# Kernel optimization log

Hardware: AMD Instinct MI355X
Metric: run time of the kernel (lower is better)

Reference implementation:

```python
import jax, jax.numpy as jnp
import numpy as np

K = 1.0        # Lorentz curvature parameter
SQRT_K = 1.0
B, E, T = 128, 64, 2048
F1, D, F2, NC = 16, 2, 32, 4


def linner(u, v):
    # Lorentz inner product <u,v>_L over the last axis (time component first)
    return -u[..., :1] * v[..., :1] + jnp.sum(u[..., 1:] * v[..., 1:], axis=-1, keepdims=True)


def add_time(space):
    # manifold.add_time / projx: time = sqrt(K + ||space||^2)
    t = jnp.sqrt(K + jnp.sum(space * space, axis=-1, keepdims=True))
    return jnp.concatenate([t, space], axis=-1)


def conv2d(x, w, padding, groups=1):
    return jax.lax.conv_general_dilated(
        x, w, window_strides=(1, 1), padding=padding,
        dimension_numbers=('NCHW', 'OIHW', 'NCHW'), feature_group_count=groups)


def bn2d(x, gamma, beta, eps=1e-3):
    # BatchNorm2d (training-mode batch statistics, eps=0.001)
    mean = jnp.mean(x, axis=(0, 2, 3), keepdims=True)
    var = jnp.var(x, axis=(0, 2, 3), keepdims=True)
    return (x - mean) * jax.lax.rsqrt(var + eps) * gamma.reshape(1, -1, 1, 1) + beta.reshape(1, -1, 1, 1)


def avgpool_w(x, k=4):
    # torch AvgPool2d((1,k), stride=k), floor mode
    Wo = x.shape[-1] // k
    return jnp.mean(x[..., :Wo * k].reshape(x.shape[:-1] + (Wo, k)), axis=-1)


def lorentz_bn(x, s, eps=1e-5):
    # AdaMom-style Riemannian batch norm on the hyperboloid (eta=1 -> pure batch stats,
    # learn_mean=False -> target mean is origin, learn_std=True -> learnable scale s).
    C = x.shape[-1]
    o = jnp.zeros((C,), x.dtype).at[0].set(SQRT_K)                      # origin
    avg = jnp.mean(x, axis=0, keepdims=True)
    mu = SQRT_K * avg / jnp.sqrt(jnp.maximum(-linner(avg, avg), 1e-8))  # batch centroid
    xin = -linner(x, mu)                                                # >= K on manifold
    dist = SQRT_K * jnp.arccosh(jnp.maximum(xin / K, 1.0 + 1e-7))
    u = x - (xin / K) * mu                                              # log_mu direction
    v = dist * u / jnp.sqrt(jnp.maximum(linner(u, u), 1e-8))            # log_mu(x)
    var = jnp.mean(dist * dist, axis=0, keepdims=True)                  # scalar dispersion
    v = v + (linner(o, v) / (K - linner(mu, o))) * (mu + o)             # PT mu -> origin
    v = v * (s.reshape(1, 1, -1, 1) / jnp.sqrt(var + eps))
    n = jnp.sqrt(jnp.maximum(linner(v, v), 1e-9))
    return jnp.cosh(n / SQRT_K) * o + SQRT_K * jnp.sinh(n / SQRT_K) * v / n  # exp_origin


def lorentz_avgpool_w(x, k=4):
    # window mean followed by Lorentz centroid renormalization
    Bb, H, W, C = x.shape
    Wo = W // k
    avg = jnp.mean(x[:, :, :Wo * k, :].reshape(Bb, H, Wo, k, C), axis=3)
    return SQRT_K * avg / jnp.sqrt(jnp.maximum(-linner(avg, avg), 1e-8))


def lorentz_flatten(x):
    Bb, H, W, C = x.shape
    t = x[..., 0].reshape(Bb, -1)
    s = x[..., 1:].reshape(Bb, -1)
    t_new = jnp.sqrt(jnp.maximum(jnp.sum(t * t, axis=-1, keepdims=True) - (H * W - 1) * K, 1e-8))
    return jnp.concatenate([t_new, s], axis=-1)


def lorentz_mlr(x, a, z):
    inv = 1.0 / SQRT_K
    norm_z = jnp.linalg.norm(z, axis=-1)                                  # (NC,)
    w_t = jnp.sinh(inv * a) * norm_z
    beta = jnp.sqrt(jnp.maximum((jnp.cosh(inv * a) * norm_z) ** 2 - w_t ** 2, 1e-8))
    alpha = -x[:, :1] * w_t[None, :] + jnp.cosh(inv * a)[None, :] * (x[:, 1:] @ z.T)
    d = SQRT_K * jnp.abs(jnp.arcsinh(inv * alpha / beta[None, :]))
    return jnp.sign(alpha) * beta[None, :] * d


def setup_inputs():
    key = jax.random.key(0)
    ks = jax.random.split(key, 8)
    Cin = F1 * D + 1   # 33
    Cout = F2 + 1      # 33
    feat = F2 * 128    # flattened space dim: W 2049 -> 512 -> 513 -> 128
    return {
        'inputs': jax.random.normal(ks[0], (B, E, T), jnp.float32),
        'domains': jax.random.randint(ks[1], (B,), 0, 4, jnp.int32),
        'conv1_w': jax.random.normal(ks[2], (F1, 1, 1, 32), jnp.float32) / np.float32(np.sqrt(32.0)),
        'bn1_gamma': jnp.ones((F1,), jnp.float32),
        'bn1_beta': jnp.zeros((F1,), jnp.float32),
        'conv2_w': jax.random.normal(ks[3], (F1 * D, 1, E, 1), jnp.float32) / np.float32(np.sqrt(E)),
        'bn2_gamma': jnp.ones((F1 * D,), jnp.float32),
        'bn2_beta': jnp.zeros((F1 * D,), jnp.float32),
        'ec1_w': jax.random.normal(ks[4], (F1 * D, 1, 1, 16), jnp.float32) / np.float32(np.sqrt(16.0)),
        'lc1_w': jax.random.normal(ks[5], (Cout, Cin), jnp.float32) / np.float32(np.sqrt(Cin)),
        'bn_s': jnp.ones((513,), jnp.float32),
        'mlr_a': jax.random.normal(ks[6], (NC,), jnp.float32) * 0.01,
        'mlr_z': jax.random.normal(ks[7], (NC, feat), jnp.float32) * 0.01,
    }


def reference(inputs, domains, conv1_w, bn1_gamma, bn1_beta, conv2_w, bn2_gamma, bn2_beta,
              ec1_w, lc1_w, bn_s, mlr_a, mlr_z):
    x = inputs[:, None, :, :]                           # (B,1,E,T)
    x = conv2d(x, conv1_w, [(0, 0), (16, 16)])          # (B,16,64,2049)
    x = bn2d(x, bn1_gamma, bn1_beta)
    x = conv2d(x, conv2_w, [(0, 0), (0, 0)], groups=F1) # (B,32,1,2049) depthwise over electrodes
    x = bn2d(x, bn2_gamma, bn2_beta)
    x = jax.nn.elu(x)
    x = avgpool_w(x)                                    # (B,32,1,512)  (dropout = eval no-op)
    x = conv2d(x, ec1_w, [(0, 0), (8, 8)], groups=F1 * D)  # (B,32,1,513)
    x = jnp.transpose(x, (0, 2, 3, 1))                  # (B,1,513,32) channels-last
    x = x / (jnp.linalg.norm(x, axis=-1, keepdims=True) + 1e-8)
    x = add_time(x)                                     # projx(pad(x, (1,0))) -> (B,1,513,33)
    # LorentzConv2d 1x1 (kernel_len=1): clamp time, linear, recompute time from space output
    pre = jnp.concatenate([jnp.maximum(x[..., :1], SQRT_K), x[..., 1:]], axis=-1)
    y = jnp.einsum('bhwi,oi->bhwo', pre, lc1_w)
    x = add_time(y[..., 1:])
    x = lorentz_bn(x, bn_s)
    x = add_time(jax.nn.elu(x[..., 1:]))                # LorentzeLU
    x = lorentz_avgpool_w(x)                            # (B,1,128,33)
    feats = lorentz_flatten(x)                          # (B, 4097)
    logits = lorentz_mlr(feats, mlr_a, mlr_z)           # (B, 4)
    return logits, feats
```

## Files before the change

kernel.cpp:

```cpp
#include <hip/hip_runtime.h>
#include <math.h>

#define BB 128
#define EE 64
#define TT 2048
#define C2 32
#define W1 2049
#define WPW 512
#define FEAT 4096
#define NBLK 1024

#define OFF_P    ((size_t)0)
#define OFF_X2   ((size_t)4194304)
#define OFF_PSUM ((size_t)8388608)
#define OFF_PSQ  ((size_t)8421376)
#define OFF_SS   ((size_t)8454144)
#define OFF_ZZ   ((size_t)8454208)
#define OFF_QSQ  ((size_t)10551360)

__device__ __forceinline__ unsigned short f2b(float f) {
    unsigned int u = __float_as_uint(f);
    u += 0x7FFFu + ((u >> 16) & 1u);
    return (unsigned short)(u >> 16);
}
__device__ __forceinline__ float b2f(unsigned short s) {
    return __uint_as_float(((unsigned int)s) << 16);
}

__global__ __launch_bounds__(256) void k_p(const float* __restrict__ in,
        const float* __restrict__ w2, unsigned short* __restrict__ P) {
    int b = blockIdx.y, t0 = blockIdx.x * 256, tid = threadIdx.x;
    __shared__ unsigned short li[64][256];
    __shared__ float lw2s[32][64];
    const float* ib = in + (size_t)b * EE * TT + t0;
    for (int j = tid; j < 64 * 64; j += 256) {
        int e = j >> 6, q = j & 63;
        float4 v = *(const float4*)(ib + e * TT + q * 4);
        li[e][q * 4 + 0] = f2b(v.x); li[e][q * 4 + 1] = f2b(v.y);
        li[e][q * 4 + 2] = f2b(v.z); li[e][q * 4 + 3] = f2b(v.w);
    }
    for (int j = tid; j < 2048; j += 256) lw2s[j >> 6][j & 63] = w2[j];
    __syncthreads();
    int cg = tid >> 6, colg = tid & 63;
    int c8 = cg * 8;
    float acc[4][8];
#pragma unroll
    for (int x = 0; x < 4; x++)
#pragma unroll
        for (int jj = 0; jj < 8; jj++) acc[x][jj] = 0.f;
    for (int e = 0; e < 64; e += 2) {
        uint2 r0 = *(const uint2*)&li[e][colg * 4];
        uint2 r1 = *(const uint2*)&li[e + 1][colg * 4];
        float v0[4], v1[4];
        v0[0] = __uint_as_float(r0.x << 16); v0[1] = __uint_as_float(r0.x & 0xFFFF0000u);
        v0[2] = __uint_as_float(r0.y << 16); v0[3] = __uint_as_float(r0.y & 0xFFFF0000u);
        v1[0] = __uint_as_float(r1.x << 16); v1[1] = __uint_as_float(r1.x & 0xFFFF0000u);
        v1[2] = __uint_as_float(r1.y << 16); v1[3] = __uint_as_float(r1.y & 0xFFFF0000u);
#pragma unroll
        for (int jj = 0; jj < 8; jj++) {
            float2 wv = *(const float2*)&lw2s[c8 + jj][e];
#pragma unroll
            for (int x = 0; x < 4; x++) {
                acc[x][jj] = fmaf(wv.x, v0[x], acc[x][jj]);
                acc[x][jj] = fmaf(wv.y, v1[x], acc[x][jj]);
            }
        }
    }
    unsigned short* Pb = P + (size_t)b * C2 * TT + t0 + colg * 4;
#pragma unroll
    for (int jj = 0; jj < 8; jj++) {
        int c = c8 + jj;
        uint2 o;
        o.x = (unsigned int)f2b(acc[0][jj]) | ((unsigned int)f2b(acc[1][jj]) << 16);
        o.y = (unsigned int)f2b(acc[2][jj]) | ((unsigned int)f2b(acc[3][jj]) << 16);
        *(uint2*)(Pb + (size_t)c * TT) = o;
    }
}

__global__ __launch_bounds__(256) void k_cs(const unsigned short* __restrict__ P,
        const float* __restrict__ w1, const float* __restrict__ g1,
        unsigned short* __restrict__ x2, float* __restrict__ psum, float* __restrict__ psq) {
    int bx = blockIdx.x, b = blockIdx.y, w0 = bx * 256, tid = threadIdx.x;
    __shared__ unsigned short lp[32][288];
    __shared__ float lw1[16][32];
    __shared__ float lds_s[32], lds_q[32];
    const unsigned short* Pb = P + (size_t)b * C2 * TT;
    for (int j = tid; j < 32 * 72; j += 256) {
        int c = j / 72, g4 = j % 72;
        int t = w0 - 16 + g4 * 4;
        uint2 v = make_uint2(0u, 0u);
        if (t >= 0 && t + 3 < TT) v = *(const uint2*)(Pb + (size_t)c * TT + t);
        *(uint2*)&lp[c][g4 * 4] = v;
    }
    for (int j = tid; j < 512; j += 256) {
        int g = j >> 5;
        float sgn = (g1[g] < 0.f) ? -1.f : 1.f;
        lw1[g][j & 31] = w1[j] * sgn;
    }
    __syncthreads();
    for (int r = 0; r < 8; r++) {
        int task = r * 256 + tid;
        int c = task >> 6;
        int wq = task & 63;
        int wbase = wq * 4;
        float win[36];
#pragma unroll
        for (int i = 0; i < 9; i++) {
            uint2 v = *(const uint2*)&lp[c][wbase + i * 4];
            win[i * 4 + 0] = __uint_as_float(v.x << 16);
            win[i * 4 + 1] = __uint_as_float(v.x & 0xFFFF0000u);
            win[i * 4 + 2] = __uint_as_float(v.y << 16);
            win[i * 4 + 3] = __uint_as_float(v.y & 0xFFFF0000u);
        }
        const float* wc = lw1[c >> 1];
        float ls = 0.f, lq = 0.f;
        float accs[4];
#pragma unroll
        for (int i = 0; i < 4; i++) {
            float acc = 0.f;
#pragma unroll
            for (int k = 0; k < 32; k++) acc = fmaf(wc[k], win[i + k], acc);
            accs[i] = acc;
            ls += acc; lq = fmaf(acc, acc, lq);
        }
        uint2 o;
        o.x = (unsigned int)f2b(accs[0]) | ((unsigned int)f2b(accs[1]) << 16);
        o.y = (unsigned int)f2b(accs[2]) | ((unsigned int)f2b(accs[3]) << 16);
        *(uint2*)(x2 + ((size_t)b * C2 + c) * TT + w0 + wbase) = o;
#pragma unroll
        for (int d = 1; d < 64; d <<= 1) {
            ls += __shfl_xor(ls, d);
            lq += __shfl_xor(lq, d);
        }
        if ((tid & 63) == 0) { lds_s[c] = ls; lds_q[c] = lq; }
    }
    __syncthreads();
    if (bx == 7 && tid < 32) {
        const float* wc = lw1[tid >> 1];
        float acc = 0.f;
#pragma unroll
        for (int k = 0; k < 16; k++) acc = fmaf(wc[k], b2f(lp[tid][256 + k]), acc);
        lds_s[tid] += acc;
        lds_q[tid] += acc * acc;
    }
    __syncthreads();
    if (tid < 32) {
        int blk = b * 8 + bx;
        psum[tid * NBLK + blk] = lds_s[tid];
        psq[tid * NBLK + blk]  = lds_q[tid];
    }
}

__global__ __launch_bounds__(64) void k_bn2fin(
        const float* __restrict__ psum, const float* __restrict__ psq,
        const float* __restrict__ gamma, const float* __restrict__ beta,
        float* __restrict__ ss) {
    int c = blockIdx.x, l = threadIdx.x;
    float s = 0.f, q = 0.f;
    for (int j = l; j < NBLK; j += 64) { s += psum[c * NBLK + j]; q += psq[c * NBLK + j]; }
#pragma unroll
    for (int d = 1; d < 64; d <<= 1) { s += __shfl_xor(s, d); q += __shfl_xor(q, d); }
    if (l == 0) {
        float n = (float)(BB * W1);
        float m = s / n;
        float var = q / n - m * m;
        float sc = gamma[c] * rsqrtf(var + 1e-3f);
        ss[c] = sc;
        ss[32 + c] = beta[c] - m * sc;
    }
}

__global__ __launch_bounds__(256) void k_mid(
        const unsigned short* __restrict__ x2, const float* __restrict__ ss,
        const float* __restrict__ ew, float* __restrict__ zz) {
    int b = blockIdx.y, w0 = blockIdx.x * 64, tid = threadIdx.x;
    __shared__ unsigned short lx[32][324];
    __shared__ float ly[32][82];
    __shared__ float lss[64];
    __shared__ float lew[32][17];
    const unsigned short* xb = x2 + (size_t)b * C2 * TT;
    int base_t = 4 * w0 - 32;
    for (int it = 0; it < 10; it++) {
        int idx = it * 256 + tid;
        int c = idx / 80, q = idx - c * 80;
        int t0 = base_t + q * 4;
        uint2 v = make_uint2(0u, 0u);
        if (t0 >= 0 && t0 <= TT - 4) v = *(const uint2*)(xb + (size_t)c * TT + t0);
        *(uint2*)&lx[c][q * 4] = v;
    }
    if (tid < 64) lss[tid] = ss[tid];
    for (int j = tid; j < 512; j += 256) lew[j >> 4][j & 15] = ew[j];
    __syncthreads();
    for (int it = 0; it < 10; it++) {
        int idx = it * 256 + tid;
        int c = idx & 31, j2 = idx >> 5;
        int ty = w0 - 8 + j2;
        float r = 0.f;
        if (ty >= 0 && ty < WPW) {
            uint2 v = *(const uint2*)&lx[c][j2 * 4];
            float sc = lss[c], sh = lss[32 + c];
            float a0 = fmaf(sc, __uint_as_float(v.x << 16), sh);
            float a1 = fmaf(sc, __uint_as_float(v.x & 0xFFFF0000u), sh);
            float a2 = fmaf(sc, __uint_as_float(v.y << 16), sh);
            float a3 = fmaf(sc, __uint_as_float(v.y & 0xFFFF0000u), sh);
            r = ((a0 > 0.f) ? a0 : expm1f(a0)) + ((a1 > 0.f) ? a1 : expm1f(a1))
              + ((a2 > 0.f) ? a2 : expm1f(a2)) + ((a3 > 0.f) ? a3 : expm1f(a3));
            r *= 0.25f;
        }
        ly[c][j2] = r;
    }
    __syncthreads();
    int c = tid & 31, wl = tid >> 5;
    float win[24];
#pragma unroll
    for (int m = 0; m < 12; m++) {
        float2 v = *(const float2*)&ly[c][wl * 8 + m * 2];
        win[m * 2] = v.x; win[m * 2 + 1] = v.y;
    }
    float wc[16];
#pragma unroll
    for (int k = 0; k < 16; k++) wc[k] = lew[c][k];
    float* zb = zz + ((size_t)(w0 + wl * 8) * BB + b) * C2 + c;
#pragma unroll
    for (int i = 0; i < 8; i++) {
        float acc = 0.f;
#pragma unroll
        for (int k = 0; k < 16; k++) acc = fmaf(wc[k], win[i + k], acc);
        zb[(size_t)i * BB * C2] = acc;
    }
}

__global__ __launch_bounds__(512) void k_tail(
        const float* __restrict__ zz, const float* __restrict__ lc1,
        const float* __restrict__ bs, float* __restrict__ outp,
        float* __restrict__ qsq) {
    int wp = blockIdx.x;
    int tid = threadIdx.x;
    int j = tid >> 7;
    int b = tid & 127;
    int w = wp * 4 + j;
    __shared__ float lws[33][32];
    __shared__ float lwt[33];
    __shared__ float wsum[4][2][33];
    __shared__ float vred[4][2];
    __shared__ float lavg[128][33];
    for (int i = tid; i < 1089; i += 512) {
        int o = i / 33, ii = i - o * 33;
        float v = lc1[i];
        if (ii == 0) lwt[o] = v; else lws[o][ii - 1] = v;
    }
    float* lz = &lavg[0][0];
    for (int i = tid; i < 128 * 33; i += 512) lz[i] = 0.f;
    __syncthreads();
    float x[33];
    {
        float xin[32];
        float ssq = 0.f;
        const float* zp = zz + ((size_t)w * BB + b) * C2;
#pragma unroll
        for (int i = 0; i < 32; i += 4) {
            float4 v = *(const float4*)(zp + i);
            xin[i] = v.x; xin[i + 1] = v.y; xin[i + 2] = v.z; xin[i + 3] = v.w;
        }
#pragma unroll
        for (int i = 0; i < 32; i++) ssq = fmaf(xin[i], xin[i], ssq);
        float inv = 1.f / (sqrtf(ssq) + 1e-8f);
        float s2 = 0.f;
#pragma unroll
        for (int i = 0; i < 32; i++) { xin[i] *= inv; s2 = fmaf(xin[i], xin[i], s2); }
        float t = sqrtf(1.f + s2);
        float pre0 = fmaxf(t, 1.f);
        float sy = 0.f;
        for (int o = 1; o < 33; o++) {
            float a = lwt[o] * pre0;
#pragma unroll
            for (int q4 = 0; q4 < 8; q4++) {
                float4 wv = *(const float4*)&lws[o][q4 * 4];
                a = fmaf(wv.x, xin[q4 * 4 + 0], a);
                a = fmaf(wv.y, xin[q4 * 4 + 1], a);
                a = fmaf(wv.z, xin[q4 * 4 + 2], a);
                a = fmaf(wv.w, xin[q4 * 4 + 3], a);
            }
            x[o] = a;
            sy = fmaf(a, a, sy);
        }
        x[0] = sqrtf(1.f + sy);
    }
    float mu[33];
#pragma unroll
    for (int ch = 0; ch < 33; ch++) {
        float s = x[ch];
        s += __shfl_xor(s, 1);  s += __shfl_xor(s, 2);  s += __shfl_xor(s, 4);
        s += __shfl_xor(s, 8);  s += __shfl_xor(s, 16); s += __shfl_xor(s, 32);
        mu[ch] = s;
    }
    int wv = b >> 6;
    if ((b & 63) == 0) {
#pragma unroll
        for (int ch = 0; ch < 33; ch++) wsum[j][wv][ch] = mu[ch];
    }
    __syncthreads();
#pragma unroll
    for (int ch = 0; ch < 33; ch++) mu[ch] = (wsum[j][0][ch] + wsum[j][1][ch]) * (1.f / 128.f);
    float a0 = mu[0], sp = 0.f;
#pragma unroll
    for (int i = 1; i < 33; i++) sp = fmaf(mu[i], mu[i], sp);
    float rd = rsqrtf(fmaxf(a0 * a0 - sp, 1e-8f));
#pragma unroll
    for (int ch = 0; ch < 33; ch++) mu[ch] *= rd;
    float xin2 = x[0] * mu[0];
#pragma unroll
    for (int i = 1; i < 33; i++) xin2 -= x[i] * mu[i];
    float dist = acoshf(fmaxf(xin2, 1.f + 1e-7f));
    float dq = dist * dist;
    dq += __shfl_xor(dq, 1);  dq += __shfl_xor(dq, 2);  dq += __shfl_xor(dq, 4);
    dq += __shfl_xor(dq, 8);  dq += __shfl_xor(dq, 16); dq += __shfl_xor(dq, 32);
    if ((b & 63) == 0) vred[j][wv] = dq;
    __syncthreads();
    float var = (vred[j][0] + vred[j][1]) * (1.f / 128.f);
#pragma unroll
    for (int ch = 0; ch < 33; ch++) x[ch] = x[ch] - xin2 * mu[ch];
    float lu = -x[0] * x[0];
#pragma unroll
    for (int i = 1; i < 33; i++) lu = fmaf(x[i], x[i], lu);
    float f = dist * rsqrtf(fmaxf(lu, 1e-8f));
#pragma unroll
    for (int ch = 0; ch < 33; ch++) x[ch] *= f;
    float corr = -x[0] / (1.f + mu[0]);
    x[0] += corr * (mu[0] + 1.f);
#pragma unroll
    for (int i = 1; i < 33; i++) x[i] = fmaf(corr, mu[i], x[i]);
    float scb = bs[w] * rsqrtf(var + 1e-5f);
#pragma unroll
    for (int ch = 0; ch < 33; ch++) x[ch] *= scb;
    float nn = -x[0] * x[0];
#pragma unroll
    for (int i = 1; i < 33; i++) nn = fmaf(x[i], x[i], nn);
    float n = sqrtf(fmaxf(nn, 1e-9f));
    float shn = sinhf(n) / n;
    float sg = 0.f;
#pragma unroll
    for (int i = 1; i < 33; i++) {
        float e = shn * x[i];
        e = (e > 0.f) ? e : expm1f(e);
        x[i] = e;
        sg = fmaf(e, e, sg);
    }
    x[0] = sqrtf(1.f + sg);
    for (int jj = 0; jj < 4; jj++) {
        if (j == jj) {
#pragma unroll
            for (int ch = 0; ch < 33; ch++) lavg[b][ch] += x[ch];
        }
        __syncthreads();
    }
    if (tid < 128) {
        int bb2 = tid;
        float avg[33];
#pragma unroll
        for (int ch = 0; ch < 33; ch++) avg[ch] = lavg[bb2][ch] * 0.25f;
        float sp2 = 0.f;
#pragma unroll
        for (int i = 1; i < 33; i++) sp2 = fmaf(avg[i], avg[i], sp2);
        float l = avg[0] * avg[0] - sp2;
        float rd2 = rsqrtf(fmaxf(l, 1e-8f));
        float q0 = avg[0] * rd2;
        float* fb = outp + 512 + (size_t)bb2 * 4097;
#pragma unroll
        for (int i = 1; i < 33; i++) fb[1 + wp * 32 + (i - 1)] = avg[i] * rd2;
        qsq[bb2 * 128 + wp] = q0 * q0;
    }
}

__global__ __launch_bounds__(256) void k_mlr2(
        const float* __restrict__ qsq, const float* __restrict__ z,
        const float* __restrict__ a, float* __restrict__ outp) {
    int b = blockIdx.x, tid = threadIdx.x;
    __shared__ float red[4][8];
    __shared__ float tnsh;
    if (tid < 64) {
        float s = qsq[b * 128 + tid] + qsq[b * 128 + 64 + tid];
#pragma unroll
        for (int d = 1; d < 64; d <<= 1) s += __shfl_xor(s, d);
        if (tid == 0) tnsh = sqrtf(fmaxf(s - 127.f, 1e-8f));
    }
    __syncthreads();
    float tn = tnsh;
    const float* fs = outp + 512 + (size_t)b * 4097 + 1;
    float sdot[4] = {0.f, 0.f, 0.f, 0.f}, sq[4] = {0.f, 0.f, 0.f, 0.f};
    for (int i = tid * 4; i < FEAT; i += 1024) {
        float f0 = fs[i], f1 = fs[i + 1], f2 = fs[i + 2], f3 = fs[i + 3];
#pragma unroll
        for (int c = 0; c < 4; c++) {
            float4 zv = *(const float4*)(z + c * FEAT + i);
            sdot[c] = fmaf(f0, zv.x, sdot[c]); sdot[c] = fmaf(f1, zv.y, sdot[c]);
            sdot[c] = fmaf(f2, zv.z, sdot[c]); sdot[c] = fmaf(f3, zv.w, sdot[c]);
            sq[c] = fmaf(zv.x, zv.x, sq[c]); sq[c] = fmaf(zv.y, zv.y, sq[c]);
            sq[c] = fmaf(zv.z, zv.z, sq[c]); sq[c] = fmaf(zv.w, zv.w, sq[c]);
        }
    }
#pragma unroll
    for (int d = 1; d < 64; d <<= 1) {
#pragma unroll
        for (int c = 0; c < 4; c++) {
            sdot[c] += __shfl_xor(sdot[c], d);
            sq[c]   += __shfl_xor(sq[c], d);
        }
    }
    int wv = tid >> 6;
    if ((tid & 63) == 0) {
#pragma unroll
        for (int c = 0; c < 4; c++) { red[wv][c] = sdot[c]; red[wv][4 + c] = sq[c]; }
    }
    __syncthreads();
    if (tid == 0) {
        outp[512 + (size_t)b * 4097] = tn;
#pragma unroll
        for (int c = 0; c < 4; c++) {
            float dot = red[0][c] + red[1][c] + red[2][c] + red[3][c];
            float qz  = red[0][4 + c] + red[1][4 + c] + red[2][4 + c] + red[3][4 + c];
            float nz = sqrtf(qz);
            float ca = coshf(a[c]), sa = sinhf(a[c]);
            float wt = sa * nz;
            float cb = ca * nz;
            float bb = sqrtf(fmaxf(cb * cb - wt * wt, 1e-8f));
            float alpha = fmaf(-tn, wt, ca * dot);
            float d = fabsf(asinhf(alpha / bb));
            float sg = (alpha > 0.f) ? 1.f : ((alpha < 0.f) ? -1.f : 0.f);
            outp[b * 4 + c] = sg * bb * d;
        }
    }
}

extern "C" void kernel_launch(void* const* d_in, const int* in_sizes, int n_in,
                              void* d_out, int out_size, void* d_ws, size_t ws_size,
                              hipStream_t stream) {
    const float* in   = (const float*)d_in[0];
    const float* w1   = (const float*)d_in[2];
    const float* g1   = (const float*)d_in[3];
    const float* w2   = (const float*)d_in[5];
    const float* g2   = (const float*)d_in[6];
    const float* b2   = (const float*)d_in[7];
    const float* ew   = (const float*)d_in[8];
    const float* lc1  = (const float*)d_in[9];
    const float* bs   = (const float*)d_in[10];
    const float* mlra = (const float*)d_in[11];
    const float* mlrz = (const float*)d_in[12];
    float* out = (float*)d_out;
    float* ws = (float*)d_ws;

    unsigned short* P  = (unsigned short*)(ws + OFF_P);
    unsigned short* X2 = (unsigned short*)(ws + OFF_X2);
    float* PSUM = ws + OFF_PSUM;
    float* PSQ  = ws + OFF_PSQ;
    float* SS   = ws + OFF_SS;
    float* ZZ   = ws + OFF_ZZ;
    float* QSQ  = ws + OFF_QSQ;

    k_p<<<dim3(8, 128), 256, 0, stream>>>(in, w2, P);
    k_cs<<<dim3(8, 128), 256, 0, stream>>>(P, w1, g1, X2, PSUM, PSQ);
    k_bn2fin<<<32, 64, 0, stream>>>(PSUM, PSQ, g2, b2, SS);
    k_mid<<<dim3(8, 128), 256, 0, stream>>>(X2, SS, ew, ZZ);
    k_tail<<<128, 512, 0, stream>>>(ZZ, lc1, bs, out, QSQ);
    k_mlr2<<<128, 256, 0, stream>>>(QSQ, mlrz, mlra, out);
}
```

Before: 208.9 us.

## Fuse channel normalization and Lorentz 1x1 conv into the mid kernel

Result: faster. 203.6 us (-2.5%).

```diff
diff --git a/kernel.cpp b/kernel.cpp
--- a/kernel.cpp
+++ b/kernel.cpp
@@ -15,8 +15,8 @@
 #define OFF_PSUM ((size_t)8388608)
 #define OFF_PSQ  ((size_t)8421376)
 #define OFF_SS   ((size_t)8454144)
-#define OFF_ZZ   ((size_t)8454208)
-#define OFF_QSQ  ((size_t)10551360)
+#define OFF_H    ((size_t)8454208)
+#define OFF_QSQ  ((size_t)10616896)
 
 __device__ __forceinline__ unsigned short f2b(float f) {
     unsigned int u = __float_as_uint(f);
@@ -172,12 +172,15 @@
 
 __global__ __launch_bounds__(256) void k_mid(
         const unsigned short* __restrict__ x2, const float* __restrict__ ss,
-        const float* __restrict__ ew, float* __restrict__ zz) {
+        const float* __restrict__ ew, const float* __restrict__ lc1,
+        float* __restrict__ H) {
     int b = blockIdx.y, w0 = blockIdx.x * 64, tid = threadIdx.x;
     __shared__ unsigned short lx[32][324];
     __shared__ float ly[32][82];
     __shared__ float lss[64];
     __shared__ float lew[32][17];
+    __shared__ float lc[1089];
+    __shared__ float lxn[8][32];
     const unsigned short* xb = x2 + (size_t)b * C2 * TT;
     int base_t = 4 * w0 - 32;
     for (int it = 0; it < 10; it++) {
@@ -190,6 +193,7 @@
     }
     if (tid < 64) lss[tid] = ss[tid];
     for (int j = tid; j < 512; j += 256) lew[j >> 4][j & 15] = ew[j];
+    for (int j = tid; j < 1089; j += 256) lc[j] = lc1[j];
     __syncthreads();
     for (int it = 0; it < 10; it++) {
         int idx = it * 256 + tid;
@@ -220,72 +224,68 @@
     float wc[16];
 #pragma unroll
     for (int k = 0; k < 16; k++) wc[k] = lew[c][k];
-    float* zb = zz + ((size_t)(w0 + wl * 8) * BB + b) * C2 + c;
+    float acc[8];
 #pragma unroll
     for (int i = 0; i < 8; i++) {
-        float acc = 0.f;
-#pragma unroll
-        for (int k = 0; k < 16; k++) acc = fmaf(wc[k], win[i + k], acc);
-        zb[(size_t)i * BB * C2] = acc;
+        float a = 0.f;
+#pragma unroll
+        for (int k = 0; k < 16; k++) a = fmaf(wc[k], win[i + k], a);
+        acc[i] = a;
+    }
+    float wt0 = lc[(c + 1) * 33];
+    float wreg[32];
+#pragma unroll
+    for (int k = 0; k < 32; k++) wreg[k] = lc[(c + 1) * 33 + 1 + k];
+    float* lrow = lxn[wl];
+#pragma unroll 1
+    for (int i = 0; i < 8; i++) {
+        float v = acc[i];
+        float ssq = v * v;
+        ssq += __shfl_xor(ssq, 1);  ssq += __shfl_xor(ssq, 2);
+        ssq += __shfl_xor(ssq, 4);  ssq += __shfl_xor(ssq, 8);
+        ssq += __shfl_xor(ssq, 16);
+        float inv = 1.f / (sqrtf(ssq) + 1e-8f);
+        float xn = v * inv;
+        float s2 = ssq * inv * inv;
+        float pre0 = fmaxf(sqrtf(1.f + s2), 1.f);
+        lrow[c] = xn;
+        float y = wt0 * pre0;
+#pragma unroll
+        for (int q = 0; q < 8; q++) {
+            float4 xv = *(const float4*)&lrow[q * 4];
+            y = fmaf(wreg[q * 4 + 0], xv.x, y);
+            y = fmaf(wreg[q * 4 + 1], xv.y, y);
+            y = fmaf(wreg[q * 4 + 2], xv.z, y);
+            y = fmaf(wreg[q * 4 + 3], xv.w, y);
+        }
+        float sy = y * y;
+        sy += __shfl_xor(sy, 1);  sy += __shfl_xor(sy, 2);
+        sy += __shfl_xor(sy, 4);  sy += __shfl_xor(sy, 8);
+        sy += __shfl_xor(sy, 16);
+        int w = w0 + wl * 8 + i;
+        float* hrow = H + ((size_t)w * BB + b) * 33;
+        hrow[1 + c] = y;
+        if (c == 0) hrow[0] = sqrtf(1.f + sy);
     }
 }
 
 __global__ __launch_bounds__(512) void k_tail(
-        const float* __restrict__ zz, const float* __restrict__ lc1,
-        const float* __restrict__ bs, float* __restrict__ outp,
-        float* __restrict__ qsq) {
+        const float* __restrict__ H, const float* __restrict__ bs,
+        float* __restrict__ outp, float* __restrict__ qsq) {
     int wp = blockIdx.x;
     int tid = threadIdx.x;
     int j = tid >> 7;
     int b = tid & 127;
     int w = wp * 4 + j;
-    __shared__ float lws[33][32];
-    __shared__ float lwt[33];
     __shared__ float wsum[4][2][33];
     __shared__ float vred[4][2];
     __shared__ float lavg[128][33];
-    for (int i = tid; i < 1089; i += 512) {
-        int o = i / 33, ii = i - o * 33;
-        float v = lc1[i];
-        if (ii == 0) lwt[o] = v; else lws[o][ii - 1] = v;
-    }
     float* lz = &lavg[0][0];
     for (int i = tid; i < 128 * 33; i += 512) lz[i] = 0.f;
-    __syncthreads();
     float x[33];
-    {
-        float xin[32];
-        float ssq = 0.f;
-        const float* zp = zz + ((size_t)w * BB + b) * C2;
-#pragma unroll
-        for (int i = 0; i < 32; i += 4) {
-            float4 v = *(const float4*)(zp + i);
-            xin[i] = v.x; xin[i + 1] = v.y; xin[i + 2] = v.z; xin[i + 3] = v.w;
-        }
-#pragma unroll
-        for (int i = 0; i < 32; i++) ssq = fmaf(xin[i], xin[i], ssq);
-        float inv = 1.f / (sqrtf(ssq) + 1e-8f);
-        float s2 = 0.f;
-#pragma unroll
-        for (int i = 0; i < 32; i++) { xin[i] *= inv; s2 = fmaf(xin[i], xin[i], s2); }
-        float t = sqrtf(1.f + s2);
-        float pre0 = fmaxf(t, 1.f);
-        float sy = 0.f;
-        for (int o = 1; o < 33; o++) {
-            float a = lwt[o] * pre0;
-#pragma unroll
-            for (int q4 = 0; q4 < 8; q4++) {
-                float4 wv = *(const float4*)&lws[o][q4 * 4];
-                a = fmaf(wv.x, xin[q4 * 4 + 0], a);
-                a = fmaf(wv.y, xin[q4 * 4 + 1], a);
-                a = fmaf(wv.z, xin[q4 * 4 + 2], a);
-                a = fmaf(wv.w, xin[q4 * 4 + 3], a);
-            }
-            x[o] = a;
-            sy = fmaf(a, a, sy);
-        }
-        x[0] = sqrtf(1.f + sy);
-    }
+    const float* hp = H + ((size_t)w * BB + b) * 33;
+#pragma unroll
+    for (int ch = 0; ch < 33; ch++) x[ch] = hp[ch];
     float mu[33];
 #pragma unroll
     for (int ch = 0; ch < 33; ch++) {
@@ -454,13 +454,13 @@
     float* PSUM = ws + OFF_PSUM;
     float* PSQ  = ws + OFF_PSQ;
     float* SS   = ws + OFF_SS;
-    float* ZZ   = ws + OFF_ZZ;
+    float* H    = ws + OFF_H;
     float* QSQ  = ws + OFF_QSQ;
 
     k_p<<<dim3(8, 128), 256, 0, stream>>>(in, w2, P);
     k_cs<<<dim3(8, 128), 256, 0, stream>>>(P, w1, g1, X2, PSUM, PSQ);
     k_bn2fin<<<32, 64, 0, stream>>>(PSUM, PSQ, g2, b2, SS);
-    k_mid<<<dim3(8, 128), 256, 0, stream>>>(X2, SS, ew, ZZ);
-    k_tail<<<128, 512, 0, stream>>>(ZZ, lc1, bs, out, QSQ);
+    k_mid<<<dim3(8, 128), 256, 0, stream>>>(X2, SS, ew, lc1, H);
+    k_tail<<<128, 512, 0, stream>>>(H, bs, out, QSQ);
     k_mlr2<<<128, 256, 0, stream>>>(QSQ, mlrz, mlra, out);
 }
```
